# Performance work log

Hardware: AMD Instinct MI355X
Metric: run time of the kernel (lower is better)

Reference implementation:

```python
import jax, jax.numpy as jnp
import numpy as np

N, E, D_IN, D_OUT, MAX_DEG = 50000, 800000, 128, 128, 64
ALPHA = 0.5


def _linear_params(key, fan_in, fan_out):
    s = 1.0 / np.sqrt(fan_in)
    kw, kb = jax.random.split(key)
    W = jax.random.uniform(kw, (fan_out, fan_in), jnp.float32, -s, s)
    b = jax.random.uniform(kb, (fan_out,), jnp.float32, -s, s)
    return W, b


def setup_inputs() -> dict:
    key = jax.random.key(0)
    ks = jax.random.split(key, 16)
    x = jax.random.normal(ks[0], (N, D_IN), jnp.float32)
    edge_index = jax.random.randint(ks[1], (2, E), 0, N, dtype=jnp.int64)
    in_degree = jax.random.randint(ks[2], (N,), 0, MAX_DEG, dtype=jnp.int64)
    out_degree = jax.random.randint(ks[3], (N,), 0, MAX_DEG, dtype=jnp.int64)
    out_deg_mask = jax.random.uniform(ks[4], (N,), jnp.float32)
    out_deg_mask_bias = jax.random.uniform(ks[5], (N,), jnp.float32)
    in_deg_mask = jax.random.uniform(ks[6], (N,), jnp.float32)
    in_deg_mask_bias = jax.random.uniform(ks[7], (N,), jnp.float32)
    W_src, b_src = _linear_params(ks[8], D_IN, D_OUT)
    W_dst, b_dst = _linear_params(ks[9], D_IN, D_OUT)
    W_out_f, b_out_f = _linear_params(ks[10], D_IN, 1)
    W_in_f, b_in_f = _linear_params(ks[11], D_IN, 1)
    W_fc, b_fc = _linear_params(ks[12], D_IN, D_OUT)
    # degree embedding tables, padding_idx=0 -> row 0 zeroed
    in_deg_table = (jax.random.normal(ks[13], (MAX_DEG, D_IN), jnp.float32)).at[0].set(0.0)
    out_deg_table = (jax.random.normal(ks[14], (MAX_DEG, D_IN), jnp.float32)).at[0].set(0.0)
    return {
        "x": x, "edge_index": edge_index,
        "in_degree": in_degree, "out_degree": out_degree,
        "out_deg_mask": out_deg_mask, "out_deg_mask_bias": out_deg_mask_bias,
        "in_deg_mask": in_deg_mask, "in_deg_mask_bias": in_deg_mask_bias,
        "W_src": W_src, "b_src": b_src, "W_dst": W_dst, "b_dst": b_dst,
        "W_out_f": W_out_f, "b_out_f": b_out_f, "W_in_f": W_in_f, "b_in_f": b_in_f,
        "W_fc": W_fc, "b_fc": b_fc,
        "in_deg_table": in_deg_table, "out_deg_table": out_deg_table,
    }


def reference(x, edge_index, in_degree, out_degree,
              out_deg_mask, out_deg_mask_bias, in_deg_mask, in_deg_mask_bias,
              W_src, b_src, W_dst, b_dst,
              W_out_f, b_out_f, W_in_f, b_in_f,
              W_fc, b_fc, in_deg_table, out_deg_table):
    n = x.shape[0]
    row, col = edge_index[0], edge_index[1]
    ones = jnp.ones(row.shape[0], x.dtype)
    # directed norm D_out^{-1/2} A D_in^{-1/2}; transpose reuses the same edge weights
    out_deg = jax.ops.segment_sum(ones, row, num_segments=n)
    in_deg = jax.ops.segment_sum(ones, col, num_segments=n)
    o_inv = jnp.where(out_deg > 0, jax.lax.rsqrt(jnp.maximum(out_deg, 1e-12)), 0.0)
    i_inv = jnp.where(in_deg > 0, jax.lax.rsqrt(jnp.maximum(in_deg, 1e-12)), 0.0)
    w = o_inv[row] * i_inv[col]  # [E]
    # adj_norm @ x and adj_t_norm @ x (SpMM via gather + segment_sum)
    out_nei = jax.ops.segment_sum(w[:, None] * x[col], row, num_segments=n)  # [N,D]
    in_nei = jax.ops.segment_sum(w[:, None] * x[row], col, num_segments=n)   # [N,D]
    # degree-gated filter
    c_out = (out_nei - x + out_deg_table[out_degree]) @ W_out_f.T + b_out_f  # [N,1]
    c_in = (in_nei - x + in_deg_table[in_degree]) @ W_in_f.T + b_in_f        # [N,1]
    C = jax.nn.softmax(jnp.concatenate([c_out, c_in], axis=1), axis=1)        # tau_softmax, tau=1
    C_out = C[:, 0:1] * out_deg_mask[:, None] + out_deg_mask_bias[:, None]
    C_in = C[:, 1:2] * in_deg_mask[:, None] + in_deg_mask_bias[:, None]
    out = (C_out * (out_nei @ W_src.T + b_src)
           + C_in * (in_nei @ W_dst.T + b_dst)
           + ALPHA * (x @ W_fc.T + b_fc))
    return out, C_in, C_out
```

## Files before the change

### kernel.cpp

```cpp
#include <hip/hip_runtime.h>

#define NN 50000
#define EE 800000
#define DD 128
#define CAP 48
#define MT 64
#define XSL 6250
#define PB 128
#define PCB (8 * PB)

typedef short short8_t __attribute__((ext_vector_type(8)));
typedef float f32x4 __attribute__((ext_vector_type(4)));
typedef float f32x2 __attribute__((ext_vector_type(2)));

__device__ __forceinline__ unsigned short f2bf(float f) {
    union { float f; unsigned int i; } v; v.f = f;
    unsigned int x = v.i;
    x += 0x7FFFu + ((x >> 16) & 1u);
    return (unsigned short)(x >> 16);
}
__device__ __forceinline__ unsigned int pack2(float a, float b) {
    return (unsigned int)f2bf(a) | ((unsigned int)f2bf(b) << 16);
}
__device__ __forceinline__ float2 bf2x2(unsigned int u) {
    union { unsigned int i; float f; } lo, hi;
    lo.i = u << 16;
    hi.i = u & 0xFFFF0000u;
    return make_float2(lo.f, hi.f);
}
__device__ __forceinline__ f32x2 bfup(unsigned int u) {
    union { unsigned int i; float f; } lo, hi;
    lo.i = u << 16;
    hi.i = u & 0xFFFF0000u;
    f32x2 r; r.x = lo.f; r.y = hi.f;
    return r;
}
__device__ __forceinline__ void pkadd(f32x2& a, f32x2 b) {
    asm("v_pk_add_f32 %0, %1, %0" : "+v"(a) : "v"(b));
}
__device__ __forceinline__ void pkfma(f32x2& a, f32x2 b, f32x2 w) {
    asm("v_pk_fma_f32 %0, %1, %2, %0" : "+v"(a) : "v"(b), "v"(w));
}
__device__ __forceinline__ void accnw(f32x2* ac, uint4 u) {
    pkadd(ac[0], bfup(u.x)); pkadd(ac[1], bfup(u.y));
    pkadd(ac[2], bfup(u.z)); pkadd(ac[3], bfup(u.w));
}
__device__ __forceinline__ void accw(f32x2* ac, uint4 u, float w) {
    f32x2 wp; wp.x = w; wp.y = w;
    pkfma(ac[0], bfup(u.x), wp); pkfma(ac[1], bfup(u.y), wp);
    pkfma(ac[2], bfup(u.z), wp); pkfma(ac[3], bfup(u.w), wp);
}

__global__ void __launch_bounds__(256) k_pc(
    const int* __restrict__ ei, int* __restrict__ cnt,
    unsigned short* __restrict__ bkt_row, unsigned short* __restrict__ bkt_col,
    const float* __restrict__ x,
    const float* __restrict__ W_src, const float* __restrict__ W_dst,
    const float* __restrict__ W_fc,
    unsigned short* __restrict__ xb, unsigned short* __restrict__ wbf)
{
    if (blockIdx.x < PCB) {
        int xcd = blockIdx.x & 7;
        int b   = blockIdx.x >> 3;
        int lo = xcd * XSL, hi = lo + XSL;
        for (int e = b * 256 + threadIdx.x; e < EE; e += PB * 256) {
            int r = ei[e];
            int c = ei[EE + e];
            if (r >= lo && r < hi) {
                int po = atomicAdd(&cnt[r], 1);
                if (po < CAP) bkt_row[(size_t)r * CAP + po] = (unsigned short)c;
            }
            if (c >= lo && c < hi) {
                int pi = atomicAdd(&cnt[NN + c], 1);
                if (pi < CAP) bkt_col[(size_t)c * CAP + pi] = (unsigned short)r;
            }
        }
    } else {
        int t = (blockIdx.x - PCB) * 256 + threadIdx.x;
        int base = t * 4;
        if (base < NN * DD) {
            float4 v = *(const float4*)(x + base);
            uint2 p; p.x = pack2(v.x, v.y); p.y = pack2(v.z, v.w);
            *(uint2*)(xb + base) = p;
        } else {
            int b2 = base - NN * DD;
            if (b2 < 3 * 16384) {
                int src = b2 >> 14;
                int off = b2 & 16383;
                const float* W = (src == 0) ? W_src : (src == 1) ? W_dst : W_fc;
                float sc = (src == 2) ? 0.5f : 1.0f;
                float4 v = *(const float4*)(W + off);
                uint2 p; p.x = pack2(v.x * sc, v.y * sc); p.y = pack2(v.z * sc, v.w * sc);
                *(uint2*)(wbf + b2) = p;
            }
        }
    }
}

__global__ void __launch_bounds__(256) k_prep(
    const int* __restrict__ cnt, const float4* __restrict__ x4,
    float* __restrict__ invb, float* __restrict__ w2, uint2* __restrict__ xs2)
{
    int t = blockIdx.x * 256 + threadIdx.x;
    if (t < 2 * NN) {
        int d = cnt[t];
        invb[t] = (d > 0) ? (1.0f / sqrtf((float)d)) : 0.0f;
    }
    if (t < NN) {
        int dd = cnt[t];
        int di = cnt[NN + t];
        float o = (dd > 0) ? (1.0f / sqrtf((float)dd)) : 0.0f;
        w2[t] = (di > 0) ? o * sqrtf((float)di) : o;
    }
    if (t < NN * 32) {
        int node = t >> 5;
        int di = cnt[NN + node];
        float s = (di > 0) ? (1.0f / sqrtf((float)di)) : 1.0f;
        float4 v = x4[t];
        uint2 p; p.x = pack2(v.x * s, v.y * s); p.y = pack2(v.z * s, v.w * s);
        xs2[t] = p;
    }
}

__global__ void __launch_bounds__(256) k_gather(
    const uint4* __restrict__ xs4, const float4* __restrict__ x4,
    const unsigned short* __restrict__ bkt_row, const unsigned short* __restrict__ bkt_col,
    const int* __restrict__ cnt,
    const float* __restrict__ o_inv, const float* __restrict__ i_inv,
    const float* __restrict__ w2,
    const int* __restrict__ in_degree, const int* __restrict__ out_degree,
    const float* __restrict__ odm, const float* __restrict__ odmb,
    const float* __restrict__ idm, const float* __restrict__ idmb,
    const float4* __restrict__ W_out_f4, const float* __restrict__ b_out_f,
    const float4* __restrict__ W_in_f4, const float* __restrict__ b_in_f,
    const float4* __restrict__ in_tab4, const float4* __restrict__ out_tab4,
    uint2* __restrict__ onb2, uint2* __restrict__ inb2,
    float* __restrict__ scbuf,
    float* __restrict__ outCin, float* __restrict__ outCout)
{
    __shared__ float4 sred[2][4][2][16][3];
    __shared__ float sg[2][2];
    __shared__ float sC[2][2];
    int half = threadIdx.x >> 7;
    int n = blockIdx.x * 2 + half;
    int t = threadIdx.x & 127;
    int g = t >> 5;
    int l = t & 31;
    int dir = g >> 1;
    int gd  = g & 1;
    int sub = l >> 4;
    int li  = l & 15;
    int shamt = gd << 4;

    const unsigned short* bp = ((dir == 0) ? bkt_row : bkt_col) + (size_t)n * CAP;
    int deg = cnt[dir * NN + n]; deg = (deg > CAP) ? CAP : deg;

    unsigned int bw = (l < 24) ? *(const unsigned int*)(bp + 2 * l) : 0u;

    float w_l = 0.0f;
    if (dir == 1) {
        unsigned int pr = __shfl(bw, l >> 1, 32);
        int il = (pr >> ((l & 1) << 4)) & 0xffff;
        if (l < deg) w_l = w2[il];
    }

    f32x2 ac[4];
    ac[0] = (f32x2)0.0f; ac[1] = (f32x2)0.0f; ac[2] = (f32x2)0.0f; ac[3] = (f32x2)0.0f;

    if (dir == 0) {
        int j = gd;
        for (; j + 14 < deg; j += 16) {
            int s0 = j + 2 * sub;
            int i0 = (__shfl(bw, s0 >> 1, 32) >> shamt) & 0xffff;
            int i1 = (__shfl(bw, (s0 + 4) >> 1, 32) >> shamt) & 0xffff;
            int i2 = (__shfl(bw, (s0 + 8) >> 1, 32) >> shamt) & 0xffff;
            int i3 = (__shfl(bw, (s0 + 12) >> 1, 32) >> shamt) & 0xffff;
            uint4 u0 = xs4[(size_t)i0 * 16 + li];
            uint4 u1 = xs4[(size_t)i1 * 16 + li];
            uint4 u2 = xs4[(size_t)i2 * 16 + li];
            uint4 u3 = xs4[(size_t)i3 * 16 + li];
            accnw(ac, u0); accnw(ac, u1); accnw(ac, u2); accnw(ac, u3);
        }
        for (; j + 6 < deg; j += 8) {
            int s0 = j + 2 * sub;
            int i0 = (__shfl(bw, s0 >> 1, 32) >> shamt) & 0xffff;
            int i1 = (__shfl(bw, (s0 + 4) >> 1, 32) >> shamt) & 0xffff;
            uint4 u0 = xs4[(size_t)i0 * 16 + li];
            uint4 u1 = xs4[(size_t)i1 * 16 + li];
            accnw(ac, u0); accnw(ac, u1);
        }
        for (; j < deg; j += 4) {
            int s0 = j + 2 * sub;
            int sc = (s0 < deg) ? s0 : gd;
            int i0 = (__shfl(bw, sc >> 1, 32) >> shamt) & 0xffff;
            if (s0 < deg) {
                uint4 u0 = xs4[(size_t)i0 * 16 + li];
                accnw(ac, u0);
            }
        }
    } else if (deg <= 32) {
        int j = gd;
        for (; j + 14 < deg; j += 16) {
            int s0 = j + 2 * sub, s1 = s0 + 4, s2 = s0 + 8, s3 = s0 + 12;
            int i0 = (__shfl(bw, s0 >> 1, 32) >> shamt) & 0xffff;
            int i1 = (__shfl(bw, s1 >> 1, 32) >> shamt) & 0xffff;
            int i2 = (__shfl(bw, s2 >> 1, 32) >> shamt) & 0xffff;
            int i3 = (__shfl(bw, s3 >> 1, 32) >> shamt) & 0xffff;
            uint4 u0 = xs4[(size_t)i0 * 16 + li];
            uint4 u1 = xs4[(size_t)i1 * 16 + li];
            uint4 u2 = xs4[(size_t)i2 * 16 + li];
            uint4 u3 = xs4[(size_t)i3 * 16 + li];
            float w0 = __shfl(w_l, s0, 32);
            float w1 = __shfl(w_l, s1, 32);
            float w2v = __shfl(w_l, s2, 32);
            float w3 = __shfl(w_l, s3, 32);
            accw(ac, u0, w0); accw(ac, u1, w1); accw(ac, u2, w2v); accw(ac, u3, w3);
        }
        for (; j + 6 < deg; j += 8) {
            int s0 = j + 2 * sub, s1 = s0 + 4;
            int i0 = (__shfl(bw, s0 >> 1, 32) >> shamt) & 0xffff;
            int i1 = (__shfl(bw, s1 >> 1, 32) >> shamt) & 0xffff;
            uint4 u0 = xs4[(size_t)i0 * 16 + li];
            uint4 u1 = xs4[(size_t)i1 * 16 + li];
            float w0 = __shfl(w_l, s0, 32);
            float w1 = __shfl(w_l, s1, 32);
            accw(ac, u0, w0); accw(ac, u1, w1);
        }
        for (; j < deg; j += 4) {
            int s0 = j + 2 * sub;
            int sc = (s0 < deg) ? s0 : gd;
            int i0 = (__shfl(bw, sc >> 1, 32) >> shamt) & 0xffff;
            float w0 = __shfl(w_l, sc, 32);
            if (s0 < deg) {
                uint4 u0 = xs4[(size_t)i0 * 16 + li];
                accw(ac, u0, w0);
            }
        }
    } else {
        for (int j = gd; j < deg; j += 4) {
            int s0 = j + 2 * sub;
            int sc = (s0 < deg) ? s0 : gd;
            int i0 = (__shfl(bw, sc >> 1, 32) >> shamt) & 0xffff;
            if (s0 < deg) {
                float w0 = w2[i0];
                uint4 u0 = xs4[(size_t)i0 * 16 + li];
                accw(ac, u0, w0);
            }
        }
    }

    sred[half][g][sub][li][0] = make_float4(ac[0].x, ac[0].y, ac[1].x, ac[1].y);
    sred[half][g][sub][li][1] = make_float4(ac[2].x, ac[2].y, ac[3].x, ac[3].y);
    __syncthreads();

    float4 r = make_float4(0.f, 0.f, 0.f, 0.f);
    if (gd == 0) {
        int src = l >> 1, q = l & 1;
        int g0 = dir * 2;
        float4 b0 = sred[half][g0][0][src][q];
        float4 b1 = sred[half][g0][1][src][q];
        float4 b2 = sred[half][g0 + 1][0][src][q];
        float4 b3 = sred[half][g0 + 1][1][src][q];
        float wn = (dir == 0) ? o_inv[n] : i_inv[n];
        r.x = wn * (b0.x + b1.x + b2.x + b3.x);
        r.y = wn * (b0.y + b1.y + b2.y + b3.y);
        r.z = wn * (b0.z + b1.z + b2.z + b3.z);
        r.w = wn * (b0.w + b1.w + b2.w + b3.w);
        float4 xv = x4[(size_t)n * 32 + l];
        float4 tb, wf;
        if (dir == 0) {
            int odg = out_degree[n];
            odg = (odg < 0) ? 0 : (odg > 63 ? 63 : odg);
            tb = out_tab4[(size_t)odg * 32 + l];
            wf = W_out_f4[l];
        } else {
            int idg = in_degree[n];
            idg = (idg < 0) ? 0 : (idg > 63 ? 63 : idg);
            tb = in_tab4[(size_t)idg * 32 + l];
            wf = W_in_f4[l];
        }
        float p = (r.x - xv.x + tb.x) * wf.x + (r.y - xv.y + tb.y) * wf.y
                + (r.z - xv.z + tb.z) * wf.z + (r.w - xv.w + tb.w) * wf.w;
        #pragma unroll
        for (int off = 16; off > 0; off >>= 1) p += __shfl_down(p, off);
        if (l == 0) sg[half][dir] = p;
    }
    __syncthreads();
    if (t == 0) {
        float c_out = sg[half][0] + b_out_f[0];
        float c_in  = sg[half][1] + b_in_f[0];
        float m  = fmaxf(c_out, c_in);
        float eo = expf(c_out - m);
        float e2 = expf(c_in  - m);
        float inv = 1.0f / (eo + e2);
        float Cout = (eo * inv) * odm[n] + odmb[n];
        float Cin  = (e2 * inv) * idm[n] + idmb[n];
        sC[half][0] = Cout; sC[half][1] = Cin;
        scbuf[2 * n]     = Cout;
        scbuf[2 * n + 1] = Cin;
        outCout[n] = Cout;
        outCin[n]  = Cin;
    }
    __syncthreads();
    if (gd == 0) {
        float C = sC[half][dir];
        uint2 pw; pw.x = pack2(C * r.x, C * r.y); pw.y = pack2(C * r.z, C * r.w);
        ((dir == 0) ? onb2 : inb2)[(size_t)n * 32 + l] = pw;
    }
}

__global__ void __launch_bounds__(256) k_gemm(
    const unsigned int* __restrict__ xb32,
    const unsigned int* __restrict__ onb32, const unsigned int* __restrict__ inb32,
    const unsigned short* __restrict__ wbf,
    const float* __restrict__ b_src, const float* __restrict__ b_dst,
    const float* __restrict__ b_fc,
    const float* __restrict__ scbuf,
    float* __restrict__ out)
{
    __shared__ unsigned short sA[MT * 72];
    __shared__ unsigned short sBt[DD * 72];

    int tid = threadIdx.x;
    int wid = tid >> 6;
    int lane = tid & 63;
    int ml = lane & 15;
    int kq = lane >> 4;
    int n0 = blockIdx.x * MT;

    f32x4 accv[8];
    #pragma unroll
    for (int i = 0; i < 8; i++) accv[i] = (f32x4)0.0f;

    const unsigned int* srcs[3] = { onb32, inb32, xb32 };

    for (int kt = 0; kt < 6; kt++) {
        int srcsel = kt >> 1;
        int k0 = (kt & 1) * 64;
        const unsigned int* S = srcs[srcsel];

        #pragma unroll
        for (int r = 0; r < 2; r++) {
            int s = tid + 256 * r;
            int row = s >> 3;
            int cg = s & 7;
            int gn = n0 + row;
            uint4 p = make_uint4(0u, 0u, 0u, 0u);
            if (gn < NN) {
                p = *(const uint4*)(S + (size_t)gn * 64 + (k0 >> 1) + cg * 4);
            }
            *(uint4*)(sA + row * 72 + cg * 8) = p;
        }
        #pragma unroll
        for (int r = 0; r < 4; r++) {
            int s = tid + 256 * r;
            int row = s >> 3;
            int cg = s & 7;
            uint4 w = *(const uint4*)(wbf + srcsel * 16384 + row * DD + k0 + cg * 8);
            *(uint4*)(sBt + row * 72 + cg * 8) = w;
        }
        __syncthreads();

        #pragma unroll
        for (int ks = 0; ks < 64; ks += 32) {
            short8_t a = *(const short8_t*)(sA + (16 * wid + ml) * 72 + ks + kq * 8);
            #pragma unroll
            for (int i = 0; i < 8; i++) {
                short8_t b = *(const short8_t*)(sBt + (16 * i + ml) * 72 + ks + kq * 8);
                accv[i] = __builtin_amdgcn_mfma_f32_16x16x32_bf16(a, b, accv[i], 0, 0, 0);
            }
        }
        __syncthreads();
    }

    int row_base = n0 + 16 * wid + 4 * kq;
    #pragma unroll
    for (int r = 0; r < 4; r++) {
        int row = row_base + r;
        if (row >= NN) continue;
        float Cout = scbuf[2 * row];
        float Cin  = scbuf[2 * row + 1];
        #pragma unroll
        for (int i = 0; i < 8; i++) {
            int col = 16 * i + ml;
            out[(size_t)row * DD + col] =
                accv[i][r] + Cout * b_src[col] + Cin * b_dst[col] + 0.5f * b_fc[col];
        }
    }
}

extern "C" void kernel_launch(void* const* d_in, const int* in_sizes, int n_in,
                              void* d_out, int out_size, void* d_ws, size_t ws_size,
                              hipStream_t stream) {
    const float* x    = (const float*)d_in[0];
    const int* ei     = (const int*)d_in[1];
    const int* in_degree  = (const int*)d_in[2];
    const int* out_degree = (const int*)d_in[3];
    const float* odm  = (const float*)d_in[4];
    const float* odmb = (const float*)d_in[5];
    const float* idm  = (const float*)d_in[6];
    const float* idmb = (const float*)d_in[7];
    const float* W_src = (const float*)d_in[8];
    const float* b_src = (const float*)d_in[9];
    const float* W_dst = (const float*)d_in[10];
    const float* b_dst = (const float*)d_in[11];
    const float* W_out_f = (const float*)d_in[12];
    const float* b_out_f = (const float*)d_in[13];
    const float* W_in_f  = (const float*)d_in[14];
    const float* b_in_f  = (const float*)d_in[15];
    const float* W_fc    = (const float*)d_in[16];
    const float* b_fc    = (const float*)d_in[17];
    const float* in_tab  = (const float*)d_in[18];
    const float* out_tab = (const float*)d_in[19];

    unsigned short* xb  = (unsigned short*)d_ws;
    unsigned short* onb = xb + (size_t)NN * DD;
    unsigned short* inb = onb + (size_t)NN * DD;
    unsigned short* xs  = inb + (size_t)NN * DD;
    float* scbuf = (float*)(xs + (size_t)NN * DD);
    float* invb  = scbuf + 2 * NN;
    float* w2    = invb + 2 * NN;
    unsigned short* wbf = (unsigned short*)(w2 + NN);
    int* cnt     = (int*)(wbf + 3 * 16384);
    unsigned short* bkt_row = (unsigned short*)(cnt + 2 * NN);
    unsigned short* bkt_col = bkt_row + (size_t)NN * CAP;

    hipMemsetAsync(cnt, 0, (size_t)2 * NN * sizeof(int), stream);

    int conv_quads = (NN * DD + 3 * 16384) / 4;
    int conv_blocks = (conv_quads + 255) / 256;
    k_pc<<<PCB + conv_blocks, 256, 0, stream>>>(ei, cnt, bkt_row, bkt_col,
                                                x, W_src, W_dst, W_fc, xb, wbf);
    k_prep<<<(NN * 32 + 255) / 256, 256, 0, stream>>>(cnt, (const float4*)x,
                                                      invb, w2, (uint2*)xs);

    float* o_inv = invb;
    float* i_inv = invb + NN;
    float* out_p  = (float*)d_out;
    float* cin_p  = out_p + (size_t)NN * DD;
    float* cout_p = cin_p + NN;

    k_gather<<<NN / 2, 256, 0, stream>>>((const uint4*)xs, (const float4*)x,
                                         bkt_row, bkt_col, cnt,
                                         o_inv, i_inv, w2, in_degree, out_degree,
                                         odm, odmb, idm, idmb,
                                         (const float4*)W_out_f, b_out_f,
                                         (const float4*)W_in_f, b_in_f,
                                         (const float4*)in_tab, (const float4*)out_tab,
                                         (uint2*)onb, (uint2*)inb,
                                         scbuf, cin_p, cout_p);

    k_gemm<<<(NN + MT - 1) / MT, 256, 0, stream>>>(
        (const unsigned int*)xb, (const unsigned int*)onb, (const unsigned int*)inb,
        wbf, b_src, b_dst, b_fc, scbuf, out_p);
}
```

Before: 275.1 us.

## Reuse scaled bf16 x in GEMM and drop separate x conversion pass

Removes the separate bf16 copy of x produced in k_pc. The GEMM now consumes the already-computed in-degree-scaled bf16 x (xs) and undoes the scaling per row with a new sinv factor, kept in a separate accumulator set. This saves a full read of x and a bf16 write, but doubles the GEMM accumulator registers, which may lower occupancy, and adds rounding error from the scaled values. It also doubles the edge-bucketing block count and uses nontemporal loads for the edge indices.

Result: slower. 286.8 us (+4.2%).

```diff
diff --git a/kernel.cpp b/kernel.cpp
--- a/kernel.cpp
+++ b/kernel.cpp
@@ -6,7 +6,7 @@
 #define CAP 48
 #define MT 64
 #define XSL 6250
-#define PB 128
+#define PB 256
 #define PCB (8 * PB)
 
 typedef short short8_t __attribute__((ext_vector_type(8)));
@@ -54,18 +54,17 @@
 __global__ void __launch_bounds__(256) k_pc(
     const int* __restrict__ ei, int* __restrict__ cnt,
     unsigned short* __restrict__ bkt_row, unsigned short* __restrict__ bkt_col,
-    const float* __restrict__ x,
     const float* __restrict__ W_src, const float* __restrict__ W_dst,
     const float* __restrict__ W_fc,
-    unsigned short* __restrict__ xb, unsigned short* __restrict__ wbf)
+    unsigned short* __restrict__ wbf)
 {
     if (blockIdx.x < PCB) {
         int xcd = blockIdx.x & 7;
         int b   = blockIdx.x >> 3;
         int lo = xcd * XSL, hi = lo + XSL;
         for (int e = b * 256 + threadIdx.x; e < EE; e += PB * 256) {
-            int r = ei[e];
-            int c = ei[EE + e];
+            int r = __builtin_nontemporal_load(ei + e);
+            int c = __builtin_nontemporal_load(ei + EE + e);
             if (r >= lo && r < hi) {
                 int po = atomicAdd(&cnt[r], 1);
                 if (po < CAP) bkt_row[(size_t)r * CAP + po] = (unsigned short)c;
@@ -77,29 +76,23 @@
         }
     } else {
         int t = (blockIdx.x - PCB) * 256 + threadIdx.x;
-        int base = t * 4;
-        if (base < NN * DD) {
-            float4 v = *(const float4*)(x + base);
-            uint2 p; p.x = pack2(v.x, v.y); p.y = pack2(v.z, v.w);
-            *(uint2*)(xb + base) = p;
-        } else {
-            int b2 = base - NN * DD;
-            if (b2 < 3 * 16384) {
-                int src = b2 >> 14;
-                int off = b2 & 16383;
-                const float* W = (src == 0) ? W_src : (src == 1) ? W_dst : W_fc;
-                float sc = (src == 2) ? 0.5f : 1.0f;
-                float4 v = *(const float4*)(W + off);
-                uint2 p; p.x = pack2(v.x * sc, v.y * sc); p.y = pack2(v.z * sc, v.w * sc);
-                *(uint2*)(wbf + b2) = p;
-            }
+        int b2 = t * 4;
+        if (b2 < 3 * 16384) {
+            int src = b2 >> 14;
+            int off = b2 & 16383;
+            const float* W = (src == 0) ? W_src : (src == 1) ? W_dst : W_fc;
+            float sc = (src == 2) ? 0.5f : 1.0f;
+            float4 v = *(const float4*)(W + off);
+            uint2 p; p.x = pack2(v.x * sc, v.y * sc); p.y = pack2(v.z * sc, v.w * sc);
+            *(uint2*)(wbf + b2) = p;
         }
     }
 }
 
 __global__ void __launch_bounds__(256) k_prep(
     const int* __restrict__ cnt, const float4* __restrict__ x4,
-    float* __restrict__ invb, float* __restrict__ w2, uint2* __restrict__ xs2)
+    float* __restrict__ invb, float* __restrict__ w2, float* __restrict__ sinv,
+    uint2* __restrict__ xs2)
 {
     int t = blockIdx.x * 256 + threadIdx.x;
     if (t < 2 * NN) {
@@ -110,7 +103,9 @@
         int dd = cnt[t];
         int di = cnt[NN + t];
         float o = (dd > 0) ? (1.0f / sqrtf((float)dd)) : 0.0f;
-        w2[t] = (di > 0) ? o * sqrtf((float)di) : o;
+        float sq = sqrtf((float)di);
+        w2[t] = (di > 0) ? o * sq : o;
+        sinv[t] = (di > 0) ? sq : 1.0f;
     }
     if (t < NN * 32) {
         int node = t >> 5;
@@ -310,12 +305,12 @@
 }
 
 __global__ void __launch_bounds__(256) k_gemm(
-    const unsigned int* __restrict__ xb32,
+    const unsigned int* __restrict__ xs32,
     const unsigned int* __restrict__ onb32, const unsigned int* __restrict__ inb32,
     const unsigned short* __restrict__ wbf,
     const float* __restrict__ b_src, const float* __restrict__ b_dst,
     const float* __restrict__ b_fc,
-    const float* __restrict__ scbuf,
+    const float* __restrict__ scbuf, const float* __restrict__ sinv,
     float* __restrict__ out)
 {
     __shared__ unsigned short sA[MT * 72];
@@ -329,10 +324,11 @@
     int n0 = blockIdx.x * MT;
 
     f32x4 accv[8];
+    f32x4 accx[8];
     #pragma unroll
-    for (int i = 0; i < 8; i++) accv[i] = (f32x4)0.0f;
-
-    const unsigned int* srcs[3] = { onb32, inb32, xb32 };
+    for (int i = 0; i < 8; i++) { accv[i] = (f32x4)0.0f; accx[i] = (f32x4)0.0f; }
+
+    const unsigned int* srcs[3] = { onb32, inb32, xs32 };
 
     for (int kt = 0; kt < 6; kt++) {
         int srcsel = kt >> 1;
@@ -361,13 +357,25 @@
         }
         __syncthreads();
 
-        #pragma unroll
-        for (int ks = 0; ks < 64; ks += 32) {
-            short8_t a = *(const short8_t*)(sA + (16 * wid + ml) * 72 + ks + kq * 8);
+        if (srcsel < 2) {
             #pragma unroll
-            for (int i = 0; i < 8; i++) {
-                short8_t b = *(const short8_t*)(sBt + (16 * i + ml) * 72 + ks + kq * 8);
-                accv[i] = __builtin_amdgcn_mfma_f32_16x16x32_bf16(a, b, accv[i], 0, 0, 0);
+            for (int ks = 0; ks < 64; ks += 32) {
+                short8_t a = *(const short8_t*)(sA + (16 * wid + ml) * 72 + ks + kq * 8);
+                #pragma unroll
+                for (int i = 0; i < 8; i++) {
+                    short8_t b = *(const short8_t*)(sBt + (16 * i + ml) * 72 + ks + kq * 8);
+                    accv[i] = __builtin_amdgcn_mfma_f32_16x16x32_bf16(a, b, accv[i], 0, 0, 0);
+                }
+            }
+        } else {
+            #pragma unroll
+            for (int ks = 0; ks < 64; ks += 32) {
+                short8_t a = *(const short8_t*)(sA + (16 * wid + ml) * 72 + ks + kq * 8);
+                #pragma unroll
+                for (int i = 0; i < 8; i++) {
+                    short8_t b = *(const short8_t*)(sBt + (16 * i + ml) * 72 + ks + kq * 8);
+                    accx[i] = __builtin_amdgcn_mfma_f32_16x16x32_bf16(a, b, accx[i], 0, 0, 0);
+                }
             }
         }
         __syncthreads();
@@ -380,11 +388,13 @@
         if (row >= NN) continue;
         float Cout = scbuf[2 * row];
         float Cin  = scbuf[2 * row + 1];
+        float si   = sinv[row];
         #pragma unroll
         for (int i = 0; i < 8; i++) {
             int col = 16 * i + ml;
             out[(size_t)row * DD + col] =
-                accv[i][r] + Cout * b_src[col] + Cin * b_dst[col] + 0.5f * b_fc[col];
+                accv[i][r] + si * accx[i][r]
+                + Cout * b_src[col] + Cin * b_dst[col] + 0.5f * b_fc[col];
         }
     }
 }
@@ -413,26 +423,25 @@
     const float* in_tab  = (const float*)d_in[18];
     const float* out_tab = (const float*)d_in[19];
 
-    unsigned short* xb  = (unsigned short*)d_ws;
-    unsigned short* onb = xb + (size_t)NN * DD;
+    unsigned short* xs  = (unsigned short*)d_ws;
+    unsigned short* onb = xs + (size_t)NN * DD;
     unsigned short* inb = onb + (size_t)NN * DD;
-    unsigned short* xs  = inb + (size_t)NN * DD;
-    float* scbuf = (float*)(xs + (size_t)NN * DD);
+    float* scbuf = (float*)(inb + (size_t)NN * DD);
     float* invb  = scbuf + 2 * NN;
     float* w2    = invb + 2 * NN;
-    unsigned short* wbf = (unsigned short*)(w2 + NN);
+    float* sinv  = w2 + NN;
+    unsigned short* wbf = (unsigned short*)(sinv + NN);
     int* cnt     = (int*)(wbf + 3 * 16384);
     unsigned short* bkt_row = (unsigned short*)(cnt + 2 * NN);
     unsigned short* bkt_col = bkt_row + (size_t)NN * CAP;
 
     hipMemsetAsync(cnt, 0, (size_t)2 * NN * sizeof(int), stream);
 
-    int conv_quads = (NN * DD + 3 * 16384) / 4;
-    int conv_blocks = (conv_quads + 255) / 256;
-    k_pc<<<PCB + conv_blocks, 256, 0, stream>>>(ei, cnt, bkt_row, bkt_col,
-                                                x, W_src, W_dst, W_fc, xb, wbf);
+    int wconv_blocks = (3 * 16384 / 4 + 255) / 256;
+    k_pc<<<PCB + wconv_blocks, 256, 0, stream>>>(ei, cnt, bkt_row, bkt_col,
+                                                 W_src, W_dst, W_fc, wbf);
     k_prep<<<(NN * 32 + 255) / 256, 256, 0, stream>>>(cnt, (const float4*)x,
-                                                      invb, w2, (uint2*)xs);
+                                                      invb, w2, sinv, (uint2*)xs);
 
     float* o_inv = invb;
     float* i_inv = invb + NN;
@@ -451,6 +460,6 @@
                                          scbuf, cin_p, cout_p);
 
     k_gemm<<<(NN + MT - 1) / MT, 256, 0, stream>>>(
-        (const unsigned int*)xb, (const unsigned int*)onb, (const unsigned int*)inb,
-        wbf, b_src, b_dst, b_fc, scbuf, out_p);
-}
+        (const unsigned int*)xs, (const unsigned int*)onb, (const unsigned int*)inb,
+        wbf, b_src, b_dst, b_fc, scbuf, sinv, out_p);
+}
```

## Overlap x@W_fc GEMM with edge bucketing and drop pre-scaled x copy

Applied to the files above, without the earlier changes.

Moves the ALPHA*x@W_fc product out of the final GEMM into extra blocks of the bucketing kernel, so it runs concurrently with the atomic edge placement and writes an fp32 xfc buffer that the final GEMM adds in its epilogue. The pre-scaled bf16 x copy (xs) and the w2 table are removed. Both gather directions now use per-neighbor weights from the inverse-sqrt tables on the plain bf16 x, which shrinks the prep kernel to a tiny k_inv. The trade-offs are an extra fp32 N×D buffer written and read, weighted FMAs instead of plain adds in the out-direction gather, and fewer placement blocks.

Measured after the change: 307.0 us. 1.12x slower.

```diff
diff --git a/kernel.cpp b/kernel.cpp
--- a/kernel.cpp
+++ b/kernel.cpp
@@ -6,8 +6,11 @@
 #define CAP 48
 #define MT 64
 #define XSL 6250
-#define PB 128
-#define PCB (8 * PB)
+#define PB 64
+#define PLACEB (8 * PB)
+#define GXB ((NN + MT - 1) / MT)
+#define WCB 32
+#define XCB (NN * DD / 1024)
 
 typedef short short8_t __attribute__((ext_vector_type(8)));
 typedef float f32x4 __attribute__((ext_vector_type(4)));
@@ -21,12 +24,6 @@
 }
 __device__ __forceinline__ unsigned int pack2(float a, float b) {
     return (unsigned int)f2bf(a) | ((unsigned int)f2bf(b) << 16);
-}
-__device__ __forceinline__ float2 bf2x2(unsigned int u) {
-    union { unsigned int i; float f; } lo, hi;
-    lo.i = u << 16;
-    hi.i = u & 0xFFFF0000u;
-    return make_float2(lo.f, hi.f);
 }
 __device__ __forceinline__ f32x2 bfup(unsigned int u) {
     union { unsigned int i; float f; } lo, hi;
@@ -35,15 +32,8 @@
     f32x2 r; r.x = lo.f; r.y = hi.f;
     return r;
 }
-__device__ __forceinline__ void pkadd(f32x2& a, f32x2 b) {
-    asm("v_pk_add_f32 %0, %1, %0" : "+v"(a) : "v"(b));
-}
 __device__ __forceinline__ void pkfma(f32x2& a, f32x2 b, f32x2 w) {
     asm("v_pk_fma_f32 %0, %1, %2, %0" : "+v"(a) : "v"(b), "v"(w));
-}
-__device__ __forceinline__ void accnw(f32x2* ac, uint4 u) {
-    pkadd(ac[0], bfup(u.x)); pkadd(ac[1], bfup(u.y));
-    pkadd(ac[2], bfup(u.z)); pkadd(ac[3], bfup(u.w));
 }
 __device__ __forceinline__ void accw(f32x2* ac, uint4 u, float w) {
     f32x2 wp; wp.x = w; wp.y = w;
@@ -57,15 +47,19 @@
     const float* __restrict__ x,
     const float* __restrict__ W_src, const float* __restrict__ W_dst,
     const float* __restrict__ W_fc,
-    unsigned short* __restrict__ xb, unsigned short* __restrict__ wbf)
+    unsigned short* __restrict__ xb, unsigned short* __restrict__ wbf,
+    float* __restrict__ xfc)
 {
-    if (blockIdx.x < PCB) {
+    __shared__ unsigned short sA[MT * 72];
+    __shared__ unsigned short sBt[DD * 72];
+
+    if (blockIdx.x < PLACEB) {
         int xcd = blockIdx.x & 7;
         int b   = blockIdx.x >> 3;
         int lo = xcd * XSL, hi = lo + XSL;
         for (int e = b * 256 + threadIdx.x; e < EE; e += PB * 256) {
-            int r = ei[e];
-            int c = ei[EE + e];
+            int r = __builtin_nontemporal_load(ei + e);
+            int c = __builtin_nontemporal_load(ei + EE + e);
             if (r >= lo && r < hi) {
                 int po = atomicAdd(&cnt[r], 1);
                 if (po < CAP) bkt_row[(size_t)r * CAP + po] = (unsigned short)c;
@@ -75,59 +69,99 @@
                 if (pi < CAP) bkt_col[(size_t)c * CAP + pi] = (unsigned short)r;
             }
         }
+    } else if (blockIdx.x < PLACEB + GXB) {
+        int tid = threadIdx.x;
+        int wid = tid >> 6;
+        int lane = tid & 63;
+        int ml = lane & 15;
+        int kq = lane >> 4;
+        int n0 = (blockIdx.x - PLACEB) * MT;
+
+        f32x4 accv[8];
+        #pragma unroll
+        for (int i = 0; i < 8; i++) accv[i] = (f32x4)0.0f;
+
+        for (int kt = 0; kt < 2; kt++) {
+            int k0 = kt * 64;
+            #pragma unroll
+            for (int r = 0; r < 4; r++) {
+                int s = tid + 256 * r;
+                int row = s >> 4;
+                int cq = s & 15;
+                int gn = n0 + row;
+                uint2 p = make_uint2(0u, 0u);
+                if (gn < NN) {
+                    float4 v = *(const float4*)(x + (size_t)gn * DD + k0 + cq * 4);
+                    p.x = pack2(v.x, v.y); p.y = pack2(v.z, v.w);
+                }
+                *(uint2*)(sA + row * 72 + cq * 4) = p;
+            }
+            #pragma unroll
+            for (int r = 0; r < 8; r++) {
+                int s = tid + 256 * r;
+                int row = s >> 4;
+                int cq = s & 15;
+                float4 v = *(const float4*)(W_fc + (size_t)row * DD + k0 + cq * 4);
+                uint2 p; p.x = pack2(0.5f * v.x, 0.5f * v.y);
+                p.y = pack2(0.5f * v.z, 0.5f * v.w);
+                *(uint2*)(sBt + row * 72 + cq * 4) = p;
+            }
+            __syncthreads();
+            #pragma unroll
+            for (int ks = 0; ks < 64; ks += 32) {
+                short8_t a = *(const short8_t*)(sA + (16 * wid + ml) * 72 + ks + kq * 8);
+                #pragma unroll
+                for (int i = 0; i < 8; i++) {
+                    short8_t b = *(const short8_t*)(sBt + (16 * i + ml) * 72 + ks + kq * 8);
+                    accv[i] = __builtin_amdgcn_mfma_f32_16x16x32_bf16(a, b, accv[i], 0, 0, 0);
+                }
+            }
+            __syncthreads();
+        }
+        int row_base = n0 + 16 * wid + 4 * kq;
+        #pragma unroll
+        for (int r = 0; r < 4; r++) {
+            int row = row_base + r;
+            if (row >= NN) continue;
+            #pragma unroll
+            for (int i = 0; i < 8; i++) {
+                xfc[(size_t)row * DD + 16 * i + ml] = accv[i][r];
+            }
+        }
+    } else if (blockIdx.x < PLACEB + GXB + WCB) {
+        int t = (blockIdx.x - PLACEB - GXB) * 256 + threadIdx.x;
+        int b2 = t * 4;
+        if (b2 < 2 * 16384) {
+            int src = b2 >> 14;
+            int off = b2 & 16383;
+            const float* W = (src == 0) ? W_src : W_dst;
+            float4 v = *(const float4*)(W + off);
+            uint2 p; p.x = pack2(v.x, v.y); p.y = pack2(v.z, v.w);
+            *(uint2*)(wbf + b2) = p;
+        }
     } else {
-        int t = (blockIdx.x - PCB) * 256 + threadIdx.x;
+        int t = (blockIdx.x - PLACEB - GXB - WCB) * 256 + threadIdx.x;
         int base = t * 4;
         if (base < NN * DD) {
             float4 v = *(const float4*)(x + base);
             uint2 p; p.x = pack2(v.x, v.y); p.y = pack2(v.z, v.w);
             *(uint2*)(xb + base) = p;
-        } else {
-            int b2 = base - NN * DD;
-            if (b2 < 3 * 16384) {
-                int src = b2 >> 14;
-                int off = b2 & 16383;
-                const float* W = (src == 0) ? W_src : (src == 1) ? W_dst : W_fc;
-                float sc = (src == 2) ? 0.5f : 1.0f;
-                float4 v = *(const float4*)(W + off);
-                uint2 p; p.x = pack2(v.x * sc, v.y * sc); p.y = pack2(v.z * sc, v.w * sc);
-                *(uint2*)(wbf + b2) = p;
-            }
-        }
-    }
-}
-
-__global__ void __launch_bounds__(256) k_prep(
-    const int* __restrict__ cnt, const float4* __restrict__ x4,
-    float* __restrict__ invb, float* __restrict__ w2, uint2* __restrict__ xs2)
-{
+        }
+    }
+}
+
+__global__ void k_inv(const int* __restrict__ cnt, float* __restrict__ inv) {
     int t = blockIdx.x * 256 + threadIdx.x;
-    if (t < 2 * NN) {
-        int d = cnt[t];
-        invb[t] = (d > 0) ? (1.0f / sqrtf((float)d)) : 0.0f;
-    }
-    if (t < NN) {
-        int dd = cnt[t];
-        int di = cnt[NN + t];
-        float o = (dd > 0) ? (1.0f / sqrtf((float)dd)) : 0.0f;
-        w2[t] = (di > 0) ? o * sqrtf((float)di) : o;
-    }
-    if (t < NN * 32) {
-        int node = t >> 5;
-        int di = cnt[NN + node];
-        float s = (di > 0) ? (1.0f / sqrtf((float)di)) : 1.0f;
-        float4 v = x4[t];
-        uint2 p; p.x = pack2(v.x * s, v.y * s); p.y = pack2(v.z * s, v.w * s);
-        xs2[t] = p;
-    }
+    if (t >= 2 * NN) return;
+    int d = cnt[t];
+    inv[t] = (d > 0) ? (1.0f / sqrtf((float)d)) : 0.0f;
 }
 
 __global__ void __launch_bounds__(256) k_gather(
-    const uint4* __restrict__ xs4, const float4* __restrict__ x4,
+    const uint4* __restrict__ xb4, const float4* __restrict__ x4,
     const unsigned short* __restrict__ bkt_row, const unsigned short* __restrict__ bkt_col,
     const int* __restrict__ cnt,
     const float* __restrict__ o_inv, const float* __restrict__ i_inv,
-    const float* __restrict__ w2,
     const int* __restrict__ in_degree, const int* __restrict__ out_degree,
     const float* __restrict__ odm, const float* __restrict__ odmb,
     const float* __restrict__ idm, const float* __restrict__ idmb,
@@ -153,52 +187,22 @@
     int shamt = gd << 4;
 
     const unsigned short* bp = ((dir == 0) ? bkt_row : bkt_col) + (size_t)n * CAP;
+    const float* wtab = (dir == 0) ? i_inv : o_inv;
     int deg = cnt[dir * NN + n]; deg = (deg > CAP) ? CAP : deg;
 
     unsigned int bw = (l < 24) ? *(const unsigned int*)(bp + 2 * l) : 0u;
 
     float w_l = 0.0f;
-    if (dir == 1) {
+    {
         unsigned int pr = __shfl(bw, l >> 1, 32);
         int il = (pr >> ((l & 1) << 4)) & 0xffff;
-        if (l < deg) w_l = w2[il];
+        if (l < deg) w_l = wtab[il];
     }
 
     f32x2 ac[4];
     ac[0] = (f32x2)0.0f; ac[1] = (f32x2)0.0f; ac[2] = (f32x2)0.0f; ac[3] = (f32x2)0.0f;
 
-    if (dir == 0) {
-        int j = gd;
-        for (; j + 14 < deg; j += 16) {
-            int s0 = j + 2 * sub;
-            int i0 = (__shfl(bw, s0 >> 1, 32) >> shamt) & 0xffff;
-            int i1 = (__shfl(bw, (s0 + 4) >> 1, 32) >> shamt) & 0xffff;
-            int i2 = (__shfl(bw, (s0 + 8) >> 1, 32) >> shamt) & 0xffff;
-            int i3 = (__shfl(bw, (s0 + 12) >> 1, 32) >> shamt) & 0xffff;
-            uint4 u0 = xs4[(size_t)i0 * 16 + li];
-            uint4 u1 = xs4[(size_t)i1 * 16 + li];
-            uint4 u2 = xs4[(size_t)i2 * 16 + li];
-            uint4 u3 = xs4[(size_t)i3 * 16 + li];
-            accnw(ac, u0); accnw(ac, u1); accnw(ac, u2); accnw(ac, u3);
-        }
-        for (; j + 6 < deg; j += 8) {
-            int s0 = j + 2 * sub;
-            int i0 = (__shfl(bw, s0 >> 1, 32) >> shamt) & 0xffff;
-            int i1 = (__shfl(bw, (s0 + 4) >> 1, 32) >> shamt) & 0xffff;
-            uint4 u0 = xs4[(size_t)i0 * 16 + li];
-            uint4 u1 = xs4[(size_t)i1 * 16 + li];
-            accnw(ac, u0); accnw(ac, u1);
-        }
-        for (; j < deg; j += 4) {
-            int s0 = j + 2 * sub;
-            int sc = (s0 < deg) ? s0 : gd;
-            int i0 = (__shfl(bw, sc >> 1, 32) >> shamt) & 0xffff;
-            if (s0 < deg) {
-                uint4 u0 = xs4[(size_t)i0 * 16 + li];
-                accnw(ac, u0);
-            }
-        }
-    } else if (deg <= 32) {
+    if (deg <= 32) {
         int j = gd;
         for (; j + 14 < deg; j += 16) {
             int s0 = j + 2 * sub, s1 = s0 + 4, s2 = s0 + 8, s3 = s0 + 12;
@@ -206,10 +210,10 @@
             int i1 = (__shfl(bw, s1 >> 1, 32) >> shamt) & 0xffff;
             int i2 = (__shfl(bw, s2 >> 1, 32) >> shamt) & 0xffff;
             int i3 = (__shfl(bw, s3 >> 1, 32) >> shamt) & 0xffff;
-            uint4 u0 = xs4[(size_t)i0 * 16 + li];
-            uint4 u1 = xs4[(size_t)i1 * 16 + li];
-            uint4 u2 = xs4[(size_t)i2 * 16 + li];
-            uint4 u3 = xs4[(size_t)i3 * 16 + li];
+            uint4 u0 = xb4[(size_t)i0 * 16 + li];
+            uint4 u1 = xb4[(size_t)i1 * 16 + li];
+            uint4 u2 = xb4[(size_t)i2 * 16 + li];
+            uint4 u3 = xb4[(size_t)i3 * 16 + li];
             float w0 = __shfl(w_l, s0, 32);
             float w1 = __shfl(w_l, s1, 32);
             float w2v = __shfl(w_l, s2, 32);
@@ -220,8 +224,8 @@
             int s0 = j + 2 * sub, s1 = s0 + 4;
             int i0 = (__shfl(bw, s0 >> 1, 32) >> shamt) & 0xffff;
             int i1 = (__shfl(bw, s1 >> 1, 32) >> shamt) & 0xffff;
-            uint4 u0 = xs4[(size_t)i0 * 16 + li];
-            uint4 u1 = xs4[(size_t)i1 * 16 + li];
+            uint4 u0 = xb4[(size_t)i0 * 16 + li];
+            uint4 u1 = xb4[(size_t)i1 * 16 + li];
             float w0 = __shfl(w_l, s0, 32);
             float w1 = __shfl(w_l, s1, 32);
             accw(ac, u0, w0); accw(ac, u1, w1);
@@ -232,7 +236,7 @@
             int i0 = (__shfl(bw, sc >> 1, 32) >> shamt) & 0xffff;
             float w0 = __shfl(w_l, sc, 32);
             if (s0 < deg) {
-                uint4 u0 = xs4[(size_t)i0 * 16 + li];
+                uint4 u0 = xb4[(size_t)i0 * 16 + li];
                 accw(ac, u0, w0);
             }
         }
@@ -242,8 +246,8 @@
             int sc = (s0 < deg) ? s0 : gd;
             int i0 = (__shfl(bw, sc >> 1, 32) >> shamt) & 0xffff;
             if (s0 < deg) {
-                float w0 = w2[i0];
-                uint4 u0 = xs4[(size_t)i0 * 16 + li];
+                float w0 = wtab[i0];
+                uint4 u0 = xb4[(size_t)i0 * 16 + li];
                 accw(ac, u0, w0);
             }
         }
@@ -310,12 +314,11 @@
 }
 
 __global__ void __launch_bounds__(256) k_gemm(
-    const unsigned int* __restrict__ xb32,
     const unsigned int* __restrict__ onb32, const unsigned int* __restrict__ inb32,
     const unsigned short* __restrict__ wbf,
     const float* __restrict__ b_src, const float* __restrict__ b_dst,
     const float* __restrict__ b_fc,
-    const float* __restrict__ scbuf,
+    const float* __restrict__ scbuf, const float* __restrict__ xfc,
     float* __restrict__ out)
 {
     __shared__ unsigned short sA[MT * 72];
@@ -332,9 +335,9 @@
     #pragma unroll
     for (int i = 0; i < 8; i++) accv[i] = (f32x4)0.0f;
 
-    const unsigned int* srcs[3] = { onb32, inb32, xb32 };
-
-    for (int kt = 0; kt < 6; kt++) {
+    const unsigned int* srcs[2] = { onb32, inb32 };
+
+    for (int kt = 0; kt < 4; kt++) {
         int srcsel = kt >> 1;
         int k0 = (kt & 1) * 64;
         const unsigned int* S = srcs[srcsel];
@@ -384,7 +387,8 @@
         for (int i = 0; i < 8; i++) {
             int col = 16 * i + ml;
             out[(size_t)row * DD + col] =
-                accv[i][r] + Cout * b_src[col] + Cin * b_dst[col] + 0.5f * b_fc[col];
+                accv[i][r] + xfc[(size_t)row * DD + col]
+                + Cout * b_src[col] + Cin * b_dst[col] + 0.5f * b_fc[col];
         }
     }
 }
@@ -416,23 +420,19 @@
     unsigned short* xb  = (unsigned short*)d_ws;
     unsigned short* onb = xb + (size_t)NN * DD;
     unsigned short* inb = onb + (size_t)NN * DD;
-    unsigned short* xs  = inb + (size_t)NN * DD;
-    float* scbuf = (float*)(xs + (size_t)NN * DD);
+    float* xfc   = (float*)(inb + (size_t)NN * DD);
+    float* scbuf = xfc + (size_t)NN * DD;
     float* invb  = scbuf + 2 * NN;
-    float* w2    = invb + 2 * NN;
-    unsigned short* wbf = (unsigned short*)(w2 + NN);
-    int* cnt     = (int*)(wbf + 3 * 16384);
+    unsigned short* wbf = (unsigned short*)(invb + 2 * NN);
+    int* cnt     = (int*)(wbf + 2 * 16384);
     unsigned short* bkt_row = (unsigned short*)(cnt + 2 * NN);
     unsigned short* bkt_col = bkt_row + (size_t)NN * CAP;
 
     hipMemsetAsync(cnt, 0, (size_t)2 * NN * sizeof(int), stream);
 
-    int conv_quads = (NN * DD + 3 * 16384) / 4;
-    int conv_blocks = (conv_quads + 255) / 256;
-    k_pc<<<PCB + conv_blocks, 256, 0, stream>>>(ei, cnt, bkt_row, bkt_col,
-                                                x, W_src, W_dst, W_fc, xb, wbf);
-    k_prep<<<(NN * 32 + 255) / 256, 256, 0, stream>>>(cnt, (const float4*)x,
-                                                      invb, w2, (uint2*)xs);
+    k_pc<<<PLACEB + GXB + WCB + XCB, 256, 0, stream>>>(
+        ei, cnt, bkt_row, bkt_col, x, W_src, W_dst, W_fc, xb, wbf, xfc);
+    k_inv<<<(2 * NN + 255) / 256, 256, 0, stream>>>(cnt, invb);
 
     float* o_inv = invb;
     float* i_inv = invb + NN;
@@ -440,9 +440,9 @@
     float* cin_p  = out_p + (size_t)NN * DD;
     float* cout_p = cin_p + NN;
 
-    k_gather<<<NN / 2, 256, 0, stream>>>((const uint4*)xs, (const float4*)x,
+    k_gather<<<NN / 2, 256, 0, stream>>>((const uint4*)xb, (const float4*)x,
                                          bkt_row, bkt_col, cnt,
-                                         o_inv, i_inv, w2, in_degree, out_degree,
+                                         o_inv, i_inv, in_degree, out_degree,
                                          odm, odmb, idm, idmb,
                                          (const float4*)W_out_f, b_out_f,
                                          (const float4*)W_in_f, b_in_f,
@@ -451,6 +451,6 @@
                                          scbuf, cin_p, cout_p);
 
     k_gemm<<<(NN + MT - 1) / MT, 256, 0, stream>>>(
-        (const unsigned int*)xb, (const unsigned int*)onb, (const unsigned int*)inb,
-        wbf, b_src, b_dst, b_fc, scbuf, out_p);
-}
+        (const unsigned int*)onb, (const unsigned int*)inb,
+        wbf, b_src, b_dst, b_fc, scbuf, xfc, out_p);
+}
```

## Remove prep kernel; compute degree normalization inline in gather from raw counts

Applied to the files above, without the earlier changes.

Drops the k_prep kernel that precomputed inverse-sqrt degree arrays and a degree-prescaled bf16 copy of x. The gather now reads the plain bf16 x and computes per-neighbor weights 1/sqrt(count) directly from the count array, for both directions. It also applies the node's own normalization inline and uses nontemporal loads for edge indices. This saves a launch and a full pass over x. In exchange the gather does extra sqrt work and count lookups per edge, and the out-direction path goes from unweighted adds to weighted FMAs.

Result: slower. 282.5 us (+2.7%).

```diff
diff --git a/kernel.cpp b/kernel.cpp
--- a/kernel.cpp
+++ b/kernel.cpp
@@ -22,12 +22,6 @@
 __device__ __forceinline__ unsigned int pack2(float a, float b) {
     return (unsigned int)f2bf(a) | ((unsigned int)f2bf(b) << 16);
 }
-__device__ __forceinline__ float2 bf2x2(unsigned int u) {
-    union { unsigned int i; float f; } lo, hi;
-    lo.i = u << 16;
-    hi.i = u & 0xFFFF0000u;
-    return make_float2(lo.f, hi.f);
-}
 __device__ __forceinline__ f32x2 bfup(unsigned int u) {
     union { unsigned int i; float f; } lo, hi;
     lo.i = u << 16;
@@ -35,15 +29,8 @@
     f32x2 r; r.x = lo.f; r.y = hi.f;
     return r;
 }
-__device__ __forceinline__ void pkadd(f32x2& a, f32x2 b) {
-    asm("v_pk_add_f32 %0, %1, %0" : "+v"(a) : "v"(b));
-}
 __device__ __forceinline__ void pkfma(f32x2& a, f32x2 b, f32x2 w) {
     asm("v_pk_fma_f32 %0, %1, %2, %0" : "+v"(a) : "v"(b), "v"(w));
-}
-__device__ __forceinline__ void accnw(f32x2* ac, uint4 u) {
-    pkadd(ac[0], bfup(u.x)); pkadd(ac[1], bfup(u.y));
-    pkadd(ac[2], bfup(u.z)); pkadd(ac[3], bfup(u.w));
 }
 __device__ __forceinline__ void accw(f32x2* ac, uint4 u, float w) {
     f32x2 wp; wp.x = w; wp.y = w;
@@ -64,8 +51,8 @@
         int b   = blockIdx.x >> 3;
         int lo = xcd * XSL, hi = lo + XSL;
         for (int e = b * 256 + threadIdx.x; e < EE; e += PB * 256) {
-            int r = ei[e];
-            int c = ei[EE + e];
+            int r = __builtin_nontemporal_load(ei + e);
+            int c = __builtin_nontemporal_load(ei + EE + e);
             if (r >= lo && r < hi) {
                 int po = atomicAdd(&cnt[r], 1);
                 if (po < CAP) bkt_row[(size_t)r * CAP + po] = (unsigned short)c;
@@ -97,37 +84,10 @@
     }
 }
 
-__global__ void __launch_bounds__(256) k_prep(
-    const int* __restrict__ cnt, const float4* __restrict__ x4,
-    float* __restrict__ invb, float* __restrict__ w2, uint2* __restrict__ xs2)
-{
-    int t = blockIdx.x * 256 + threadIdx.x;
-    if (t < 2 * NN) {
-        int d = cnt[t];
-        invb[t] = (d > 0) ? (1.0f / sqrtf((float)d)) : 0.0f;
-    }
-    if (t < NN) {
-        int dd = cnt[t];
-        int di = cnt[NN + t];
-        float o = (dd > 0) ? (1.0f / sqrtf((float)dd)) : 0.0f;
-        w2[t] = (di > 0) ? o * sqrtf((float)di) : o;
-    }
-    if (t < NN * 32) {
-        int node = t >> 5;
-        int di = cnt[NN + node];
-        float s = (di > 0) ? (1.0f / sqrtf((float)di)) : 1.0f;
-        float4 v = x4[t];
-        uint2 p; p.x = pack2(v.x * s, v.y * s); p.y = pack2(v.z * s, v.w * s);
-        xs2[t] = p;
-    }
-}
-
 __global__ void __launch_bounds__(256) k_gather(
-    const uint4* __restrict__ xs4, const float4* __restrict__ x4,
+    const uint4* __restrict__ xb4, const float4* __restrict__ x4,
     const unsigned short* __restrict__ bkt_row, const unsigned short* __restrict__ bkt_col,
     const int* __restrict__ cnt,
-    const float* __restrict__ o_inv, const float* __restrict__ i_inv,
-    const float* __restrict__ w2,
     const int* __restrict__ in_degree, const int* __restrict__ out_degree,
     const float* __restrict__ odm, const float* __restrict__ odmb,
     const float* __restrict__ idm, const float* __restrict__ idmb,
@@ -153,52 +113,23 @@
     int shamt = gd << 4;
 
     const unsigned short* bp = ((dir == 0) ? bkt_row : bkt_col) + (size_t)n * CAP;
-    int deg = cnt[dir * NN + n]; deg = (deg > CAP) ? CAP : deg;
+    const int* wcnt = (dir == 0) ? (cnt + NN) : cnt;
+    int rawdeg = cnt[dir * NN + n];
+    int deg = (rawdeg > CAP) ? CAP : rawdeg;
 
     unsigned int bw = (l < 24) ? *(const unsigned int*)(bp + 2 * l) : 0u;
 
     float w_l = 0.0f;
-    if (dir == 1) {
+    {
         unsigned int pr = __shfl(bw, l >> 1, 32);
         int il = (pr >> ((l & 1) << 4)) & 0xffff;
-        if (l < deg) w_l = w2[il];
+        if (l < deg) w_l = 1.0f / sqrtf((float)wcnt[il]);
     }
 
     f32x2 ac[4];
     ac[0] = (f32x2)0.0f; ac[1] = (f32x2)0.0f; ac[2] = (f32x2)0.0f; ac[3] = (f32x2)0.0f;
 
-    if (dir == 0) {
-        int j = gd;
-        for (; j + 14 < deg; j += 16) {
-            int s0 = j + 2 * sub;
-            int i0 = (__shfl(bw, s0 >> 1, 32) >> shamt) & 0xffff;
-            int i1 = (__shfl(bw, (s0 + 4) >> 1, 32) >> shamt) & 0xffff;
-            int i2 = (__shfl(bw, (s0 + 8) >> 1, 32) >> shamt) & 0xffff;
-            int i3 = (__shfl(bw, (s0 + 12) >> 1, 32) >> shamt) & 0xffff;
-            uint4 u0 = xs4[(size_t)i0 * 16 + li];
-            uint4 u1 = xs4[(size_t)i1 * 16 + li];
-            uint4 u2 = xs4[(size_t)i2 * 16 + li];
-            uint4 u3 = xs4[(size_t)i3 * 16 + li];
-            accnw(ac, u0); accnw(ac, u1); accnw(ac, u2); accnw(ac, u3);
-        }
-        for (; j + 6 < deg; j += 8) {
-            int s0 = j + 2 * sub;
-            int i0 = (__shfl(bw, s0 >> 1, 32) >> shamt) & 0xffff;
-            int i1 = (__shfl(bw, (s0 + 4) >> 1, 32) >> shamt) & 0xffff;
-            uint4 u0 = xs4[(size_t)i0 * 16 + li];
-            uint4 u1 = xs4[(size_t)i1 * 16 + li];
-            accnw(ac, u0); accnw(ac, u1);
-        }
-        for (; j < deg; j += 4) {
-            int s0 = j + 2 * sub;
-            int sc = (s0 < deg) ? s0 : gd;
-            int i0 = (__shfl(bw, sc >> 1, 32) >> shamt) & 0xffff;
-            if (s0 < deg) {
-                uint4 u0 = xs4[(size_t)i0 * 16 + li];
-                accnw(ac, u0);
-            }
-        }
-    } else if (deg <= 32) {
+    if (deg <= 32) {
         int j = gd;
         for (; j + 14 < deg; j += 16) {
             int s0 = j + 2 * sub, s1 = s0 + 4, s2 = s0 + 8, s3 = s0 + 12;
@@ -206,10 +137,10 @@
             int i1 = (__shfl(bw, s1 >> 1, 32) >> shamt) & 0xffff;
             int i2 = (__shfl(bw, s2 >> 1, 32) >> shamt) & 0xffff;
             int i3 = (__shfl(bw, s3 >> 1, 32) >> shamt) & 0xffff;
-            uint4 u0 = xs4[(size_t)i0 * 16 + li];
-            uint4 u1 = xs4[(size_t)i1 * 16 + li];
-            uint4 u2 = xs4[(size_t)i2 * 16 + li];
-            uint4 u3 = xs4[(size_t)i3 * 16 + li];
+            uint4 u0 = xb4[(size_t)i0 * 16 + li];
+            uint4 u1 = xb4[(size_t)i1 * 16 + li];
+            uint4 u2 = xb4[(size_t)i2 * 16 + li];
+            uint4 u3 = xb4[(size_t)i3 * 16 + li];
             float w0 = __shfl(w_l, s0, 32);
             float w1 = __shfl(w_l, s1, 32);
             float w2v = __shfl(w_l, s2, 32);
@@ -220,8 +151,8 @@
             int s0 = j + 2 * sub, s1 = s0 + 4;
             int i0 = (__shfl(bw, s0 >> 1, 32) >> shamt) & 0xffff;
             int i1 = (__shfl(bw, s1 >> 1, 32) >> shamt) & 0xffff;
-            uint4 u0 = xs4[(size_t)i0 * 16 + li];
-            uint4 u1 = xs4[(size_t)i1 * 16 + li];
+            uint4 u0 = xb4[(size_t)i0 * 16 + li];
+            uint4 u1 = xb4[(size_t)i1 * 16 + li];
             float w0 = __shfl(w_l, s0, 32);
             float w1 = __shfl(w_l, s1, 32);
             accw(ac, u0, w0); accw(ac, u1, w1);
@@ -232,7 +163,7 @@
             int i0 = (__shfl(bw, sc >> 1, 32) >> shamt) & 0xffff;
             float w0 = __shfl(w_l, sc, 32);
             if (s0 < deg) {
-                uint4 u0 = xs4[(size_t)i0 * 16 + li];
+                uint4 u0 = xb4[(size_t)i0 * 16 + li];
                 accw(ac, u0, w0);
             }
         }
@@ -242,8 +173,8 @@
             int sc = (s0 < deg) ? s0 : gd;
             int i0 = (__shfl(bw, sc >> 1, 32) >> shamt) & 0xffff;
             if (s0 < deg) {
-                float w0 = w2[i0];
-                uint4 u0 = xs4[(size_t)i0 * 16 + li];
+                float w0 = 1.0f / sqrtf((float)wcnt[i0]);
+                uint4 u0 = xb4[(size_t)i0 * 16 + li];
                 accw(ac, u0, w0);
             }
         }
@@ -261,7 +192,7 @@
         float4 b1 = sred[half][g0][1][src][q];
         float4 b2 = sred[half][g0 + 1][0][src][q];
         float4 b3 = sred[half][g0 + 1][1][src][q];
-        float wn = (dir == 0) ? o_inv[n] : i_inv[n];
+        float wn = (rawdeg > 0) ? (1.0f / sqrtf((float)rawdeg)) : 0.0f;
         r.x = wn * (b0.x + b1.x + b2.x + b3.x);
         r.y = wn * (b0.y + b1.y + b2.y + b3.y);
         r.z = wn * (b0.z + b1.z + b2.z + b3.z);
@@ -416,11 +347,8 @@
     unsigned short* xb  = (unsigned short*)d_ws;
     unsigned short* onb = xb + (size_t)NN * DD;
     unsigned short* inb = onb + (size_t)NN * DD;
-    unsigned short* xs  = inb + (size_t)NN * DD;
-    float* scbuf = (float*)(xs + (size_t)NN * DD);
-    float* invb  = scbuf + 2 * NN;
-    float* w2    = invb + 2 * NN;
-    unsigned short* wbf = (unsigned short*)(w2 + NN);
+    float* scbuf = (float*)(inb + (size_t)NN * DD);
+    unsigned short* wbf = (unsigned short*)(scbuf + 2 * NN);
     int* cnt     = (int*)(wbf + 3 * 16384);
     unsigned short* bkt_row = (unsigned short*)(cnt + 2 * NN);
     unsigned short* bkt_col = bkt_row + (size_t)NN * CAP;
@@ -431,18 +359,14 @@
     int conv_blocks = (conv_quads + 255) / 256;
     k_pc<<<PCB + conv_blocks, 256, 0, stream>>>(ei, cnt, bkt_row, bkt_col,
                                                 x, W_src, W_dst, W_fc, xb, wbf);
-    k_prep<<<(NN * 32 + 255) / 256, 256, 0, stream>>>(cnt, (const float4*)x,
-                                                      invb, w2, (uint2*)xs);
-
-    float* o_inv = invb;
-    float* i_inv = invb + NN;
+
     float* out_p  = (float*)d_out;
     float* cin_p  = out_p + (size_t)NN * DD;
     float* cout_p = cin_p + NN;
 
-    k_gather<<<NN / 2, 256, 0, stream>>>((const uint4*)xs, (const float4*)x,
+    k_gather<<<NN / 2, 256, 0, stream>>>((const uint4*)xb, (const float4*)x,
                                          bkt_row, bkt_col, cnt,
-                                         o_inv, i_inv, w2, in_degree, out_degree,
+                                         in_degree, out_degree,
                                          odm, odmb, idm, idmb,
                                          (const float4*)W_out_f, b_out_f,
                                          (const float4*)W_in_f, b_in_f,
```
